# Optimization experiments

Hardware: AMD Instinct MI355X
Metric: run time of the kernel (lower is better)

Reference implementation:

```python
import jax, jax.numpy as jnp
import numpy as np

B = 4096
IND = 512
OUTD = 512
DEG = 2
P = 2  # dim_treat
KNOTS = [[0.33, 0.66], [0.33, 0.66]]
D = DEG + 1 + len(KNOTS[0])  # 5 basis functions per treatment dim


def setup_inputs() -> dict:
    key = jax.random.key(0)
    k1, k2, k3 = jax.random.split(key, 3)
    x = jax.random.uniform(k1, (B, P + IND), dtype=jnp.float32)  # treat dims in [0,1]
    weight = jax.random.uniform(k2, (IND, OUTD, D ** P), dtype=jnp.float32)  # torch.rand init
    bias = jax.random.uniform(k3, (OUTD, D ** P), dtype=jnp.float32)
    return {"x": x, "weight": weight, "bias": bias}


def _truncated_power_basis(x_treat):
    # x_treat: [B, P] -> basis: [B, P, D]
    knots = jnp.asarray(KNOTS, dtype=x_treat.dtype)  # [P, n_knots]
    # polynomial part: 1, x, x^2, ... x^DEG
    pows = jnp.stack([x_treat ** i for i in range(DEG + 1)], axis=-1)  # [B, P, DEG+1]
    # truncated part: relu(x - knot)^DEG  (DEG > 1 branch of original code)
    trunc = jax.nn.relu(x_treat[:, :, None] - knots[None, :, :]) ** DEG  # [B, P, n_knots]
    return jnp.concatenate([pows, trunc], axis=-1)


def reference(x, weight, bias):
    x_treat = x[:, :P]          # [B, P]
    x_feature = x[:, P:]        # [B, IND]
    basis = _truncated_power_basis(x_treat)  # [B, P, D]
    # Kronecker product across the two treatment dims: outer product, flattened
    kb = jnp.einsum('bi,bj->bij', basis[:, 0, :], basis[:, 1, :]).reshape(x.shape[0], D * P * 0 + D * D)  # [B, D^2]
    # fused: (weight^T @ x_feature) contracted with the per-sample basis coefficients
    out = jnp.einsum('bi,iod,bd->bo', x_feature, weight, kb)  # [B, OUTD]
    out = out + kb @ bias.T      # bias also varies with treatment basis
    out = jax.nn.relu(out)       # act='relu'
    # islastlayer=0: re-attach treatment dims
    return jnp.concatenate([x_treat, out], axis=1)  # [B, P + OUTD]
```

## Files before the change

### kernel.cpp

```cpp
#include <hip/hip_runtime.h>
#include <hip/hip_bf16.h>
#include <string.h>

#define NB    4096
#define IND_  512
#define OUTD_ 512
#define XCOLS 514
#define ND    25
#define KTOT  12800

#define WT_DS   262144
#define WT_BIAS 6553600

#define BM 32
#define BN 128

#define PWI 64
#define PWO 4
#define PWC (PWO * ND)
#define T8P 112

typedef float  f32x4  __attribute__((ext_vector_type(4)));
typedef int    i32x4  __attribute__((ext_vector_type(4)));
typedef int    i32x8  __attribute__((ext_vector_type(8)));
typedef unsigned int   u32x2 __attribute__((ext_vector_type(2)));

__device__ __forceinline__ unsigned char f2fp8(float v) {
  if (v < 0.015625f) {
    return (unsigned char)__float2int_rn(v * 512.0f);
  }
  unsigned int u = __float_as_uint(v);
  u += 0x7ffffu + ((u >> 20) & 1u);
  int e = (int)(u >> 23) - 127 + 7;
  unsigned int m = (u >> 20) & 7u;
  return (unsigned char)((e << 3) | m);
}

__device__ __forceinline__ float basis_f(float t, int j) {
  switch (j) {
    case 0: return 1.0f;
    case 1: return t;
    case 2: return t * t;
    case 3: { float r = t - 0.33f; r = r > 0.0f ? r : 0.0f; return r * r; }
    default:{ float r = t - 0.66f; r = r > 0.0f ? r : 0.0f; return r * r; }
  }
}

__global__ __launch_bounds__(256) void prep_all_kernel(
    const float* __restrict__ x, const float* __restrict__ W,
    const float* __restrict__ bias, unsigned char* __restrict__ Xf8,
    float* __restrict__ kbKV, unsigned char* __restrict__ kbT8,
    unsigned char* __restrict__ Wt, float* __restrict__ out)
{
  __shared__ unsigned char tile8[PWI * T8P];
  const int bid = blockIdx.x;
  const int tid = threadIdx.x;

  if (bid < 512) {
    const int lane = tid & 63;
    #pragma unroll
    for (int rr = 0; rr < 2; ++rr) {
      const int b = bid * 8 + (tid >> 6) * 2 + rr;
      const float* xr = x + (size_t)b * XCOLS;
      const float* fp = xr + 2 + lane * 8;
      float2 a0 = *(const float2*)(fp + 0);
      float2 a1 = *(const float2*)(fp + 2);
      float2 a2 = *(const float2*)(fp + 4);
      float2 a3 = *(const float2*)(fp + 6);
      float xf[8] = {a0.x, a0.y, a1.x, a1.y, a2.x, a2.y, a3.x, a3.y};
      u32x2 pk;
      pk[0] = (unsigned int)f2fp8(xf[0]) | ((unsigned int)f2fp8(xf[1]) << 8) |
              ((unsigned int)f2fp8(xf[2]) << 16) | ((unsigned int)f2fp8(xf[3]) << 24);
      pk[1] = (unsigned int)f2fp8(xf[4]) | ((unsigned int)f2fp8(xf[5]) << 8) |
              ((unsigned int)f2fp8(xf[6]) << 16) | ((unsigned int)f2fp8(xf[7]) << 24);
      *reinterpret_cast<u32x2*>(Xf8 + (size_t)b * IND_ + lane * 8) = pk;

      float t0 = xr[0], t1 = xr[1];
      if (lane < 2) out[(size_t)b * XCOLS + lane] = (lane == 0) ? t0 : t1;
      {
        int d1 = lane / 5, d2 = lane - d1 * 5;
        float kvd = basis_f(t0, d1) * basis_f(t1, d2);
        if (lane < ND) {
          int bt = b >> 7, bl = b & 15, nf = (b >> 4) & 7;
          kbKV[(((size_t)lane * 32 + bt) * 16 + bl) * 8 + nf] = kvd;
        }
      }
      {
        int ta = 2 * lane, tb = 2 * lane + 1;
        unsigned char ba = 0, bb = 0;
        if (ta < ND) { int d1 = ta / 5, d2 = ta - d1 * 5;
                       ba = f2fp8(basis_f(t0, d1) * basis_f(t1, d2)); }
        if (tb < ND) { int d1 = tb / 5, d2 = tb - d1 * 5;
                       bb = f2fp8(basis_f(t0, d1) * basis_f(t1, d2)); }
        *(unsigned short*)(kbT8 + (size_t)b * 128 + 2 * lane) =
            (unsigned short)ba | ((unsigned short)bb << 8);
      }
    }
  } else {
    const int pw = bid - 512;
    const int i0 = (pw & 7) * PWI;
    const int o0 = (pw >> 3) * PWO;

    for (int t = tid; t < PWI * (PWC / 4); t += 256) {
      int il = t / (PWC / 4);
      int c4 = t - il * (PWC / 4);
      float4 v = *(const float4*)(W + ((size_t)(i0 + il) * OUTD_ + o0) * ND + c4 * 4);
      unsigned int pk = (unsigned int)f2fp8(v.x) | ((unsigned int)f2fp8(v.y) << 8) |
                        ((unsigned int)f2fp8(v.z) << 16) | ((unsigned int)f2fp8(v.w) << 24);
      *(unsigned int*)&tile8[il * T8P + c4 * 4] = pk;
    }
    __syncthreads();

    for (int g = tid; g < PWC * (PWI / 8); g += 256) {
      int c  = g >> 3;
      int ig = g & 7;
      int d  = c % 25;
      int o_l = c / 25;
      unsigned long long v = 0;
      #pragma unroll
      for (int jj = 0; jj < 8; ++jj)
        v |= (unsigned long long)tile8[(ig * 8 + jj) * T8P + c] << (8 * jj);
      int o  = o0 + o_l;
      int ib = i0 + ig * 8;
      int iw = ib >> 7;
      int wb = ib & 127;
      size_t dest = (((size_t)d * 32 + (o >> 4)) * 4 + iw) * 2048
                  + (size_t)(((wb >> 5) * 16 + (o & 15)) * 32 + (wb & 31));
      *reinterpret_cast<unsigned long long*>(Wt + dest) = v;
    }

    if ((pw & 7) == 0) {
      int o = o0 + (tid >> 6);
      int p = tid & 63;
      int ta = 2 * p, tb = 2 * p + 1;
      unsigned char ba = (ta < ND) ? f2fp8(bias[o * ND + ta]) : (unsigned char)0;
      unsigned char bb = (tb < ND) ? f2fp8(bias[o * ND + tb]) : (unsigned char)0;
      size_t dest = WT_BIAS + (size_t)(o >> 4) * 2048
                  + (size_t)(((ta >> 5) * 16 + (o & 15)) * 32 + (ta & 31));
      *(unsigned short*)(Wt + dest) =
          (unsigned short)ba | ((unsigned short)bb << 8);
    }
  }
}

__global__ __launch_bounds__(256, 3) void gemm_out_kernel(
    const unsigned char* __restrict__ Wt, const unsigned char* __restrict__ Xf8,
    const float* __restrict__ kbKV, const unsigned char* __restrict__ kbT8,
    float* __restrict__ out)
{
  const int tid  = threadIdx.x;
  const int lane = tid & 63;
  const int w    = tid >> 6;
  const int l15  = lane & 15;
  const int quad = lane >> 4;

  const int id = blockIdx.x;
  const int ox = ((id & 7) << 1) | ((id >> 3) & 1);
  const int by = id >> 4;

  const int o0 = ox * BM;
  const int b0 = by * BN;

  const int og = ox * 2 + (w >> 1);
  const int bh = w & 1;

  auto load8 = [](const unsigned char* p) -> i32x8 {
    i32x4 lo = *reinterpret_cast<const i32x4*>(p);
    i32x4 hi = *reinterpret_cast<const i32x4*>(p + 16);
    i32x8 v;
    v[0] = lo[0]; v[1] = lo[1]; v[2] = lo[2]; v[3] = lo[3];
    v[4] = hi[0]; v[5] = hi[1]; v[6] = hi[2]; v[7] = hi[3];
    return v;
  };

  f32x4 fin[4];
  #pragma unroll
  for (int nf = 0; nf < 4; ++nf) fin[nf] = (f32x4)0.0f;

  const f32x4 Z = (f32x4)0.0f;
  const float* dBase = kbKV + (((size_t)by * 16 + l15) * 8) + bh * 4;

  for (int iw = 0; iw < 4; ++iw) {
    i32x8 bfr[4];
    #pragma unroll
    for (int nf = 0; nf < 4; ++nf)
      bfr[nf] = load8(Xf8 + (size_t)(b0 + bh * 64 + nf * 16 + l15) * IND_
                          + iw * 128 + quad * 32);

    const unsigned char* aP = Wt + ((size_t)og * 4 + iw) * 2048 + lane * 32;
    const float* dP = dBase;

    f32x4 accA[4], accB[4];
    auto mfma4A = [&](const i32x8& a) {
      #pragma unroll
      for (int nf = 0; nf < 4; ++nf)
        accA[nf] = __builtin_amdgcn_mfma_scale_f32_16x16x128_f8f6f4(
            a, bfr[nf], Z, 0, 0, 0, 0x7f7f7f7f, 0, 0x7f7f7f7f);
    };
    auto mfma4B = [&](const i32x8& a) {
      #pragma unroll
      for (int nf = 0; nf < 4; ++nf)
        accB[nf] = __builtin_amdgcn_mfma_scale_f32_16x16x128_f8f6f4(
            a, bfr[nf], Z, 0, 0, 0, 0x7f7f7f7f, 0, 0x7f7f7f7f);
    };
    auto flushA = [&](const f32x4& q) {
      #pragma unroll
      for (int nf = 0; nf < 4; ++nf)
        #pragma unroll
        for (int r = 0; r < 4; ++r)
          fin[nf][r] += q[nf] * accA[nf][r];
    };
    auto flushB = [&](const f32x4& q) {
      #pragma unroll
      for (int nf = 0; nf < 4; ++nf)
        #pragma unroll
        for (int r = 0; r < 4; ++r)
          fin[nf][r] += q[nf] * accB[nf][r];
    };

    i32x8 a0 = load8(aP);
    i32x8 a1 = load8(aP + WT_DS);
    f32x4 qA = *reinterpret_cast<const f32x4*>(dP);
    f32x4 qB = *reinterpret_cast<const f32x4*>(dP + 4096);

    mfma4A(a0);
    a0 = load8(aP + 2 * WT_DS);

    for (int p = 0; p < 12; ++p) {
      mfma4B(a1);
      a1 = load8(aP + 3 * WT_DS);
      f32x4 qC = *reinterpret_cast<const f32x4*>(dP + 2 * 4096);
      flushA(qA);
      mfma4A(a0);
      a0 = load8(aP + 4 * WT_DS);
      f32x4 qD = *reinterpret_cast<const f32x4*>(dP + 3 * 4096);
      flushB(qB);
      qA = qC; qB = qD;
      aP += 2 * WT_DS;
      dP += 2 * 4096;
    }
    flushA(qA);
  }

  {
    i32x8 ab = load8(Wt + WT_BIAS + (size_t)og * 2048 + lane * 32);
    i32x8 bft[4];
    #pragma unroll
    for (int nf = 0; nf < 4; ++nf)
      bft[nf] = load8(kbT8 + (size_t)(b0 + bh * 64 + nf * 16 + l15) * 128
                           + quad * 32);
    #pragma unroll
    for (int nf = 0; nf < 4; ++nf)
      fin[nf] = __builtin_amdgcn_mfma_scale_f32_16x16x128_f8f6f4(
          ab, bft[nf], fin[nf], 0, 0, 0, 0x7f7f7f7f, 0, 0x7f7f7f7f);
  }

  #pragma unroll
  for (int nf = 0; nf < 4; ++nf) {
    int bg = b0 + bh * 64 + nf * 16 + l15;
    int oo = o0 + (w >> 1) * 16 + quad * 4;
    float* op = out + (size_t)bg * XCOLS + 2 + oo;
    float2 lo, hi;
    lo.x = fin[nf][0] > 0.0f ? fin[nf][0] : 0.0f;
    lo.y = fin[nf][1] > 0.0f ? fin[nf][1] : 0.0f;
    hi.x = fin[nf][2] > 0.0f ? fin[nf][2] : 0.0f;
    hi.y = fin[nf][3] > 0.0f ? fin[nf][3] : 0.0f;
    *(float2*)op = lo;
    *(float2*)(op + 2) = hi;
  }
}

extern "C" void kernel_launch(void* const* d_in, const int* in_sizes, int n_in,
                              void* d_out, int out_size, void* d_ws, size_t ws_size,
                              hipStream_t stream) {
  const float* x    = (const float*)d_in[0];
  const float* W    = (const float*)d_in[1];
  const float* bias = (const float*)d_in[2];
  float* out = (float*)d_out;
  char* ws = (char*)d_ws;

  const size_t xf_off  = 0;
  const size_t wf_off  = 2097152;
  const size_t kb_off  = wf_off + 6619136;
  const size_t kbt_off = kb_off + 409600;
  unsigned char* Xf8  = (unsigned char*)(ws + xf_off);
  unsigned char* Wt   = (unsigned char*)(ws + wf_off);
  float* kbKV         = (float*)(ws + kb_off);
  unsigned char* kbT8 = (unsigned char*)(ws + kbt_off);

  prep_all_kernel<<<1536, 256, 0, stream>>>(x, W, bias, Xf8, kbKV, kbT8, Wt, out);
  gemm_out_kernel<<<512, 256, 0, stream>>>(Wt, Xf8, kbKV, kbT8, out);
}
```

Baseline: 118.4 us.

## Halve output tile per block and double grid size for gemm kernel

Shrinks each block's output-dimension tile from 32 to 16 columns so all four waves share one weight group and each wave owns 32 batch rows. The grid doubles to 1024 blocks, giving more parallelism and lower per-thread register use. In exchange, weight fetches are no longer shared across waves within a block, so total weight traffic from cache rises.

```diff
diff --git a/kernel.cpp b/kernel.cpp
--- a/kernel.cpp
+++ b/kernel.cpp
@@ -12,7 +12,7 @@
 #define WT_DS   262144
 #define WT_BIAS 6553600
 
-#define BM 32
+#define BM 16
 #define BN 128
 
 #define PWI 64
@@ -155,14 +155,11 @@
   const int quad = lane >> 4;
 
   const int id = blockIdx.x;
-  const int ox = ((id & 7) << 1) | ((id >> 3) & 1);
-  const int by = id >> 4;
-
-  const int o0 = ox * BM;
+  const int og = ((id & 7) << 2) | ((id >> 3) & 3);
+  const int by = id >> 5;
+
   const int b0 = by * BN;
-
-  const int og = ox * 2 + (w >> 1);
-  const int bh = w & 1;
+  const int bq = b0 + w * 32;
 
   auto load8 = [](const unsigned char* p) -> i32x8 {
     i32x4 lo = *reinterpret_cast<const i32x4*>(p);
@@ -173,67 +170,67 @@
     return v;
   };
 
-  f32x4 fin[4];
+  f32x4 fin[2];
   #pragma unroll
-  for (int nf = 0; nf < 4; ++nf) fin[nf] = (f32x4)0.0f;
+  for (int nf = 0; nf < 2; ++nf) fin[nf] = (f32x4)0.0f;
 
   const f32x4 Z = (f32x4)0.0f;
-  const float* dBase = kbKV + (((size_t)by * 16 + l15) * 8) + bh * 4;
+  const float* dBase = kbKV + (size_t)by * 128 + l15 * 8 + w * 2;
 
   for (int iw = 0; iw < 4; ++iw) {
-    i32x8 bfr[4];
-    #pragma unroll
-    for (int nf = 0; nf < 4; ++nf)
-      bfr[nf] = load8(Xf8 + (size_t)(b0 + bh * 64 + nf * 16 + l15) * IND_
+    i32x8 bfr[2];
+    #pragma unroll
+    for (int nf = 0; nf < 2; ++nf)
+      bfr[nf] = load8(Xf8 + (size_t)(bq + nf * 16 + l15) * IND_
                           + iw * 128 + quad * 32);
 
     const unsigned char* aP = Wt + ((size_t)og * 4 + iw) * 2048 + lane * 32;
     const float* dP = dBase;
 
-    f32x4 accA[4], accB[4];
-    auto mfma4A = [&](const i32x8& a) {
-      #pragma unroll
-      for (int nf = 0; nf < 4; ++nf)
+    f32x4 accA[2], accB[2];
+    auto mfma2A = [&](const i32x8& a) {
+      #pragma unroll
+      for (int nf = 0; nf < 2; ++nf)
         accA[nf] = __builtin_amdgcn_mfma_scale_f32_16x16x128_f8f6f4(
             a, bfr[nf], Z, 0, 0, 0, 0x7f7f7f7f, 0, 0x7f7f7f7f);
     };
-    auto mfma4B = [&](const i32x8& a) {
-      #pragma unroll
-      for (int nf = 0; nf < 4; ++nf)
+    auto mfma2B = [&](const i32x8& a) {
+      #pragma unroll
+      for (int nf = 0; nf < 2; ++nf)
         accB[nf] = __builtin_amdgcn_mfma_scale_f32_16x16x128_f8f6f4(
             a, bfr[nf], Z, 0, 0, 0, 0x7f7f7f7f, 0, 0x7f7f7f7f);
     };
-    auto flushA = [&](const f32x4& q) {
-      #pragma unroll
-      for (int nf = 0; nf < 4; ++nf)
-        #pragma unroll
-        for (int r = 0; r < 4; ++r)
-          fin[nf][r] += q[nf] * accA[nf][r];
-    };
-    auto flushB = [&](const f32x4& q) {
-      #pragma unroll
-      for (int nf = 0; nf < 4; ++nf)
-        #pragma unroll
-        for (int r = 0; r < 4; ++r)
-          fin[nf][r] += q[nf] * accB[nf][r];
+    auto flushA = [&](const float2& q) {
+      #pragma unroll
+      for (int r = 0; r < 4; ++r) {
+        fin[0][r] += q.x * accA[0][r];
+        fin[1][r] += q.y * accA[1][r];
+      }
+    };
+    auto flushB = [&](const float2& q) {
+      #pragma unroll
+      for (int r = 0; r < 4; ++r) {
+        fin[0][r] += q.x * accB[0][r];
+        fin[1][r] += q.y * accB[1][r];
+      }
     };
 
     i32x8 a0 = load8(aP);
     i32x8 a1 = load8(aP + WT_DS);
-    f32x4 qA = *reinterpret_cast<const f32x4*>(dP);
-    f32x4 qB = *reinterpret_cast<const f32x4*>(dP + 4096);
-
-    mfma4A(a0);
+    float2 qA = *reinterpret_cast<const float2*>(dP);
+    float2 qB = *reinterpret_cast<const float2*>(dP + 4096);
+
+    mfma2A(a0);
     a0 = load8(aP + 2 * WT_DS);
 
     for (int p = 0; p < 12; ++p) {
-      mfma4B(a1);
+      mfma2B(a1);
       a1 = load8(aP + 3 * WT_DS);
-      f32x4 qC = *reinterpret_cast<const f32x4*>(dP + 2 * 4096);
+      float2 qC = *reinterpret_cast<const float2*>(dP + 2 * 4096);
       flushA(qA);
-      mfma4A(a0);
+      mfma2A(a0);
       a0 = load8(aP + 4 * WT_DS);
-      f32x4 qD = *reinterpret_cast<const f32x4*>(dP + 3 * 4096);
+      float2 qD = *reinterpret_cast<const float2*>(dP + 3 * 4096);
       flushB(qB);
       qA = qC; qB = qD;
       aP += 2 * WT_DS;
@@ -244,21 +241,20 @@
 
   {
     i32x8 ab = load8(Wt + WT_BIAS + (size_t)og * 2048 + lane * 32);
-    i32x8 bft[4];
-    #pragma unroll
-    for (int nf = 0; nf < 4; ++nf)
-      bft[nf] = load8(kbT8 + (size_t)(b0 + bh * 64 + nf * 16 + l15) * 128
-                           + quad * 32);
-    #pragma unroll
-    for (int nf = 0; nf < 4; ++nf)
+    i32x8 bft[2];
+    #pragma unroll
+    for (int nf = 0; nf < 2; ++nf)
+      bft[nf] = load8(kbT8 + (size_t)(bq + nf * 16 + l15) * 128 + quad * 32);
+    #pragma unroll
+    for (int nf = 0; nf < 2; ++nf)
       fin[nf] = __builtin_amdgcn_mfma_scale_f32_16x16x128_f8f6f4(
           ab, bft[nf], fin[nf], 0, 0, 0, 0x7f7f7f7f, 0, 0x7f7f7f7f);
   }
 
   #pragma unroll
-  for (int nf = 0; nf < 4; ++nf) {
-    int bg = b0 + bh * 64 + nf * 16 + l15;
-    int oo = o0 + (w >> 1) * 16 + quad * 4;
+  for (int nf = 0; nf < 2; ++nf) {
+    int bg = bq + nf * 16 + l15;
+    int oo = og * 16 + quad * 4;
     float* op = out + (size_t)bg * XCOLS + 2 + oo;
     float2 lo, hi;
     lo.x = fin[nf][0] > 0.0f ? fin[nf][0] : 0.0f;
@@ -289,5 +285,5 @@
   unsigned char* kbT8 = (unsigned char*)(ws + kbt_off);
 
   prep_all_kernel<<<1536, 256, 0, stream>>>(x, W, bias, Xf8, kbKV, kbT8, Wt, out);
-  gemm_out_kernel<<<512, 256, 0, stream>>>(Wt, Xf8, kbKV, kbT8, out);
-}
+  gemm_out_kernel<<<1024, 256, 0, stream>>>(Wt, Xf8, kbKV, kbT8, out);
+}
```

New measurement: 133.3 us. +12.6%, slower.

## Deepen GEMM MFMA/flush pipeline to three stages and batch prep loads

Applied to the files above, without the earlier changes.

In the main GEMM, the per-basis MFMA-then-scale loop is restructured from a two-accumulator to a three-accumulator rotation. Weight and basis-coefficient loads are issued further ahead, so more MFMA latency is hidden behind the flushes. Launch bounds drop from 3 to 2 blocks per SM, freeing registers for the extra accumulators at the cost of occupancy. In the prep kernel, both rows' loads and all W tile loads are issued up front before conversion, to raise memory-level parallelism.

```diff
diff --git a/kernel.cpp b/kernel.cpp
--- a/kernel.cpp
+++ b/kernel.cpp
@@ -58,16 +58,23 @@
 
   if (bid < 512) {
     const int lane = tid & 63;
-    #pragma unroll
-    for (int rr = 0; rr < 2; ++rr) {
-      const int b = bid * 8 + (tid >> 6) * 2 + rr;
-      const float* xr = x + (size_t)b * XCOLS;
-      const float* fp = xr + 2 + lane * 8;
-      float2 a0 = *(const float2*)(fp + 0);
-      float2 a1 = *(const float2*)(fp + 2);
-      float2 a2 = *(const float2*)(fp + 4);
-      float2 a3 = *(const float2*)(fp + 6);
-      float xf[8] = {a0.x, a0.y, a1.x, a1.y, a2.x, a2.y, a3.x, a3.y};
+    const int bb = bid * 8 + (tid >> 6) * 2;
+    const float* xr0 = x + (size_t)bb * XCOLS;
+    const float* xr1 = xr0 + XCOLS;
+    const float* fp0 = xr0 + 2 + lane * 8;
+    const float* fp1 = xr1 + 2 + lane * 8;
+
+    float2 c0[4], c1[4];
+    #pragma unroll
+    for (int j = 0; j < 4; ++j) c0[j] = *(const float2*)(fp0 + 2 * j);
+    #pragma unroll
+    for (int j = 0; j < 4; ++j) c1[j] = *(const float2*)(fp1 + 2 * j);
+    float t00 = xr0[0], t01 = xr0[1];
+    float t10 = xr1[0], t11 = xr1[1];
+
+    auto do_row = [&](int b, const float2* a, float t0, float t1) {
+      float xf[8] = {a[0].x, a[0].y, a[1].x, a[1].y,
+                     a[2].x, a[2].y, a[3].x, a[3].y};
       u32x2 pk;
       pk[0] = (unsigned int)f2fp8(xf[0]) | ((unsigned int)f2fp8(xf[1]) << 8) |
               ((unsigned int)f2fp8(xf[2]) << 16) | ((unsigned int)f2fp8(xf[3]) << 24);
@@ -75,7 +82,6 @@
               ((unsigned int)f2fp8(xf[6]) << 16) | ((unsigned int)f2fp8(xf[7]) << 24);
       *reinterpret_cast<u32x2*>(Xf8 + (size_t)b * IND_ + lane * 8) = pk;
 
-      float t0 = xr[0], t1 = xr[1];
       if (lane < 2) out[(size_t)b * XCOLS + lane] = (lane == 0) ? t0 : t1;
       {
         int d1 = lane / 5, d2 = lane - d1 * 5;
@@ -87,26 +93,47 @@
       }
       {
         int ta = 2 * lane, tb = 2 * lane + 1;
-        unsigned char ba = 0, bb = 0;
+        unsigned char ba = 0, bbb = 0;
         if (ta < ND) { int d1 = ta / 5, d2 = ta - d1 * 5;
                        ba = f2fp8(basis_f(t0, d1) * basis_f(t1, d2)); }
         if (tb < ND) { int d1 = tb / 5, d2 = tb - d1 * 5;
-                       bb = f2fp8(basis_f(t0, d1) * basis_f(t1, d2)); }
+                       bbb = f2fp8(basis_f(t0, d1) * basis_f(t1, d2)); }
         *(unsigned short*)(kbT8 + (size_t)b * 128 + 2 * lane) =
-            (unsigned short)ba | ((unsigned short)bb << 8);
+            (unsigned short)ba | ((unsigned short)bbb << 8);
       }
-    }
+    };
+    do_row(bb, c0, t00, t01);
+    do_row(bb + 1, c1, t10, t11);
   } else {
     const int pw = bid - 512;
     const int i0 = (pw & 7) * PWI;
     const int o0 = (pw >> 3) * PWO;
 
-    for (int t = tid; t < PWI * (PWC / 4); t += 256) {
-      int il = t / (PWC / 4);
-      int c4 = t - il * (PWC / 4);
-      float4 v = *(const float4*)(W + ((size_t)(i0 + il) * OUTD_ + o0) * ND + c4 * 4);
-      unsigned int pk = (unsigned int)f2fp8(v.x) | ((unsigned int)f2fp8(v.y) << 8) |
-                        ((unsigned int)f2fp8(v.z) << 16) | ((unsigned int)f2fp8(v.w) << 24);
+    float4 vv[7];
+    #pragma unroll
+    for (int k = 0; k < 6; ++k) {
+      int t = tid + k * 256;
+      int il = t / 25, c4 = t - il * 25;
+      vv[k] = *(const float4*)(W + ((size_t)(i0 + il) * OUTD_ + o0) * ND + c4 * 4);
+    }
+    if (tid < 64) {
+      int t = tid + 1536;
+      int il = t / 25, c4 = t - il * 25;
+      vv[6] = *(const float4*)(W + ((size_t)(i0 + il) * OUTD_ + o0) * ND + c4 * 4);
+    }
+    #pragma unroll
+    for (int k = 0; k < 6; ++k) {
+      int t = tid + k * 256;
+      int il = t / 25, c4 = t - il * 25;
+      unsigned int pk = (unsigned int)f2fp8(vv[k].x) | ((unsigned int)f2fp8(vv[k].y) << 8) |
+                        ((unsigned int)f2fp8(vv[k].z) << 16) | ((unsigned int)f2fp8(vv[k].w) << 24);
+      *(unsigned int*)&tile8[il * T8P + c4 * 4] = pk;
+    }
+    if (tid < 64) {
+      int t = tid + 1536;
+      int il = t / 25, c4 = t - il * 25;
+      unsigned int pk = (unsigned int)f2fp8(vv[6].x) | ((unsigned int)f2fp8(vv[6].y) << 8) |
+                        ((unsigned int)f2fp8(vv[6].z) << 16) | ((unsigned int)f2fp8(vv[6].w) << 24);
       *(unsigned int*)&tile8[il * T8P + c4 * 4] = pk;
     }
     __syncthreads();
@@ -134,16 +161,16 @@
       int p = tid & 63;
       int ta = 2 * p, tb = 2 * p + 1;
       unsigned char ba = (ta < ND) ? f2fp8(bias[o * ND + ta]) : (unsigned char)0;
-      unsigned char bb = (tb < ND) ? f2fp8(bias[o * ND + tb]) : (unsigned char)0;
+      unsigned char bbb = (tb < ND) ? f2fp8(bias[o * ND + tb]) : (unsigned char)0;
       size_t dest = WT_BIAS + (size_t)(o >> 4) * 2048
                   + (size_t)(((ta >> 5) * 16 + (o & 15)) * 32 + (ta & 31));
       *(unsigned short*)(Wt + dest) =
-          (unsigned short)ba | ((unsigned short)bb << 8);
-    }
-  }
-}
-
-__global__ __launch_bounds__(256, 3) void gemm_out_kernel(
+          (unsigned short)ba | ((unsigned short)bbb << 8);
+    }
+  }
+}
+
+__global__ __launch_bounds__(256, 2) void gemm_out_kernel(
     const unsigned char* __restrict__ Wt, const unsigned char* __restrict__ Xf8,
     const float* __restrict__ kbKV, const unsigned char* __restrict__ kbT8,
     float* __restrict__ out)
@@ -190,56 +217,69 @@
     const unsigned char* aP = Wt + ((size_t)og * 4 + iw) * 2048 + lane * 32;
     const float* dP = dBase;
 
-    f32x4 accA[4], accB[4];
-    auto mfma4A = [&](const i32x8& a) {
+    f32x4 accA[4], accB[4], accC[4];
+    auto mfmaA = [&](const i32x8& a) {
       #pragma unroll
       for (int nf = 0; nf < 4; ++nf)
         accA[nf] = __builtin_amdgcn_mfma_scale_f32_16x16x128_f8f6f4(
             a, bfr[nf], Z, 0, 0, 0, 0x7f7f7f7f, 0, 0x7f7f7f7f);
     };
-    auto mfma4B = [&](const i32x8& a) {
+    auto mfmaB = [&](const i32x8& a) {
       #pragma unroll
       for (int nf = 0; nf < 4; ++nf)
         accB[nf] = __builtin_amdgcn_mfma_scale_f32_16x16x128_f8f6f4(
             a, bfr[nf], Z, 0, 0, 0, 0x7f7f7f7f, 0, 0x7f7f7f7f);
     };
+    auto mfmaC = [&](const i32x8& a) {
+      #pragma unroll
+      for (int nf = 0; nf < 4; ++nf)
+        accC[nf] = __builtin_amdgcn_mfma_scale_f32_16x16x128_f8f6f4(
+            a, bfr[nf], Z, 0, 0, 0, 0x7f7f7f7f, 0, 0x7f7f7f7f);
+    };
     auto flushA = [&](const f32x4& q) {
       #pragma unroll
       for (int nf = 0; nf < 4; ++nf)
         #pragma unroll
-        for (int r = 0; r < 4; ++r)
-          fin[nf][r] += q[nf] * accA[nf][r];
+        for (int r = 0; r < 4; ++r) fin[nf][r] += q[nf] * accA[nf][r];
     };
     auto flushB = [&](const f32x4& q) {
       #pragma unroll
       for (int nf = 0; nf < 4; ++nf)
         #pragma unroll
-        for (int r = 0; r < 4; ++r)
-          fin[nf][r] += q[nf] * accB[nf][r];
+        for (int r = 0; r < 4; ++r) fin[nf][r] += q[nf] * accB[nf][r];
+    };
+    auto flushC = [&](const f32x4& q) {
+      #pragma unroll
+      for (int nf = 0; nf < 4; ++nf)
+        #pragma unroll
+        for (int r = 0; r < 4; ++r) fin[nf][r] += q[nf] * accC[nf][r];
     };
 
     i32x8 a0 = load8(aP);
     i32x8 a1 = load8(aP + WT_DS);
-    f32x4 qA = *reinterpret_cast<const f32x4*>(dP);
-    f32x4 qB = *reinterpret_cast<const f32x4*>(dP + 4096);
-
-    mfma4A(a0);
-    a0 = load8(aP + 2 * WT_DS);
-
-    for (int p = 0; p < 12; ++p) {
-      mfma4B(a1);
-      a1 = load8(aP + 3 * WT_DS);
-      f32x4 qC = *reinterpret_cast<const f32x4*>(dP + 2 * 4096);
-      flushA(qA);
-      mfma4A(a0);
-      a0 = load8(aP + 4 * WT_DS);
-      f32x4 qD = *reinterpret_cast<const f32x4*>(dP + 3 * 4096);
-      flushB(qB);
-      qA = qC; qB = qD;
-      aP += 2 * WT_DS;
-      dP += 2 * 4096;
-    }
-    flushA(qA);
+    i32x8 a2 = load8(aP + 2 * WT_DS);
+    f32x4 q0 = *reinterpret_cast<const f32x4*>(dP);
+    f32x4 q1 = *reinterpret_cast<const f32x4*>(dP + 4096);
+    f32x4 q2 = *reinterpret_cast<const f32x4*>(dP + 2 * 4096);
+
+    mfmaA(a0); a0 = load8(aP + 3 * WT_DS);
+    mfmaB(a1); a1 = load8(aP + 4 * WT_DS);
+
+    for (int p = 0; p < 7; ++p) {
+      mfmaC(a2); a2 = load8(aP + 5 * WT_DS);
+      flushA(q0); q0 = *reinterpret_cast<const f32x4*>(dP + 3 * 4096);
+      mfmaA(a0); a0 = load8(aP + 6 * WT_DS);
+      flushB(q1); q1 = *reinterpret_cast<const f32x4*>(dP + 4 * 4096);
+      mfmaB(a1); a1 = load8(aP + 7 * WT_DS);
+      flushC(q2); q2 = *reinterpret_cast<const f32x4*>(dP + 5 * 4096);
+      aP += 3 * WT_DS;
+      dP += 3 * 4096;
+    }
+    mfmaC(a2); flushA(q0);
+    mfmaA(a0); flushB(q1);
+    flushC(q2);
+    f32x4 q24 = *reinterpret_cast<const f32x4*>(dP + 3 * 4096);
+    flushA(q24);
   }
 
   {
```

New measurement: 113.5 us. 4.1% less time.
